# Performance work log

Measured on AMD Instinct MI355X. Metric: run time of the kernel, lower is better.

Reference implementation:

```python
import jax, jax.numpy as jnp
import numpy as np

T, B, D, H, O = 128, 256, 512, 1024, 1


def setup_inputs() -> dict:
    key = jax.random.key(0)
    ks = jax.random.split(key, 10)
    s_in = 1.0 / np.sqrt(D)
    s_h = 1.0 / np.sqrt(H)
    u = lambda k, shape, s: jax.random.uniform(k, shape, jnp.float32, -s, s)
    return {
        "inputs": jax.random.normal(ks[0], (T, B, D), jnp.float32),
        "hidden_state": jnp.zeros((1, B, H), jnp.float32),
        "cell_state": jnp.zeros((1, B, H), jnp.float32),
        "W1": u(ks[1], (H, D), s_in),
        "b1": u(ks[2], (H,), s_in),
        "W_ih": u(ks[3], (4 * H, H), s_h),
        "W_hh": u(ks[4], (4 * H, H), s_h),
        "b_ih": u(ks[5], (4 * H,), s_h),
        "b_hh": u(ks[6], (4 * H,), s_h),
        "W_out": u(ks[7], (O, H), s_h),
        "b_out": u(ks[8], (O,), s_h),
    }


def reference(inputs, hidden_state, cell_state, W1, b1, W_ih, W_hh, b_ih, b_hh, W_out, b_out):
    # first_layer + ReLU (dropout is identity in eval mode)
    x = jax.nn.relu(jnp.einsum("tbd,hd->tbh", inputs, W1) + b1)  # (T,B,H)
    # Precompute input contribution to all gates for every timestep.
    xg = jnp.einsum("tbh,gh->tbg", x, W_ih) + b_ih + b_hh  # (T,B,4H)
    h0 = hidden_state[0]
    c0 = cell_state[0]

    def step(carry, xg_t):
        h, c = carry
        g = xg_t + h @ W_hh.T  # (B,4H), PyTorch gate order i,f,g,o
        i, f, gg, o = jnp.split(g, 4, axis=-1)
        i = jax.nn.sigmoid(i)
        f = jax.nn.sigmoid(f)
        gg = jnp.tanh(gg)
        o = jax.nn.sigmoid(o)
        c = f * c + i * gg
        h = o * jnp.tanh(c)
        return (h, c), h

    (hT, cT), hs = jax.lax.scan(step, (h0, c0), xg)
    out = jnp.einsum("tbh,oh->tbo", hs, W_out) + b_out  # (T,B,O)
    return out, hT[None], cT[None]
```

## Files before the change

### kernel.cpp

```cpp
#include <hip/hip_runtime.h>
#include <hip/hip_bf16.h>
#include <math.h>


#define T_STEPS 128
#define BATCH   256
#define DIM     512
#define HID     1024
#define GATES   4096
#define FPAD    32

typedef __attribute__((ext_vector_type(8))) short short8;
typedef __attribute__((ext_vector_type(4))) float f4;
typedef __attribute__((ext_vector_type(4))) int i4;

__device__ __forceinline__ short f2bf(float f) {
    union { float f; unsigned u; } x; x.f = f;
    unsigned r = (x.u + 0x7fffu + ((x.u >> 16) & 1u)) >> 16;
    return (short)r;
}
__device__ __forceinline__ float bf2f(short s) {
    union { unsigned u; float f; } x; x.u = ((unsigned)(unsigned short)s) << 16;
    return x.f;
}
__device__ __forceinline__ float sigm(float x) { return 1.f / (1.f + __expf(-x)); }
__device__ __forceinline__ float tanh_fast(float x) { return 2.f / (1.f + __expf(-2.f * x)) - 1.f; }

__device__ __forceinline__ void gll16(const void* g, void* l) {
    __builtin_amdgcn_global_load_lds(
        (const __attribute__((address_space(1))) void*)g,
        (__attribute__((address_space(3))) void*)l, 16, 0, 0);
}
__device__ __forceinline__ void store16_wt(void* p, i4 v) {
    asm volatile("global_store_dwordx4 %0, %1, off sc0 sc1"
                 :: "v"(p), "v"(v) : "memory");
}

__global__ __launch_bounds__(256) void cvt_f32_bf16(const float* __restrict__ in,
                                                    short* __restrict__ out, int n4) {
    int i = blockIdx.x * 256 + threadIdx.x;
    if (i < n4) {
        float4 v = ((const float4*)in)[i];
        union { short s[4]; long long ll; } r;
        r.s[0] = f2bf(v.x); r.s[1] = f2bf(v.y); r.s[2] = f2bf(v.z); r.s[3] = f2bf(v.w);
        ((long long*)out)[i] = r.ll;
    }
}

__global__ __launch_bounds__(256) void cvt_h0_blocked(const float* __restrict__ h0,
                                                      short* __restrict__ dst) {
    int b = blockIdx.x, k0 = threadIdx.x * 4;
    float4 v = *(const float4*)&h0[(size_t)b * HID + k0];
    union { short s[4]; long long ll; } p;
    p.s[0] = f2bf(v.x); p.s[1] = f2bf(v.y); p.s[2] = f2bf(v.z); p.s[3] = f2bf(v.w);
    *(long long*)&dst[(k0 >> 3) * (BATCH * 8) + b * 8 + (k0 & 7)] = p.ll;
}

__global__ __launch_bounds__(256) void cvt_permute_rows(const float* __restrict__ in,
                                                        short* __restrict__ out) {
    int r = blockIdx.x;
    int hc = r >> 2, g = r & 3;
    const float* src = in + (size_t)(g * HID + hc) * HID;
    short* dst = out + (size_t)r * HID;
    int c = threadIdx.x * 4;
    float4 v = *(const float4*)&src[c];
    union { short s[4]; long long ll; } p;
    p.s[0] = f2bf(v.x); p.s[1] = f2bf(v.y); p.s[2] = f2bf(v.z); p.s[3] = f2bf(v.w);
    *(long long*)&dst[c] = p.ll;
}

__global__ __launch_bounds__(256) void bias_sum_perm(const float* __restrict__ a,
                                                     const float* __restrict__ b,
                                                     float* __restrict__ o) {
    int r = blockIdx.x * 256 + threadIdx.x;
    int hc = r >> 2, g = r & 3;
    int src = g * HID + hc;
    o[r] = a[src] + b[src];
}

__global__ __launch_bounds__(256) void copy_f32v4(const float* __restrict__ in,
                                                  float* __restrict__ out, int n4) {
    int i = blockIdx.x * 256 + threadIdx.x;
    if (i < n4) ((float4*)out)[i] = ((const float4*)in)[i];
}

__global__ __launch_bounds__(256) void zero_i32(int* __restrict__ p, int n) {
    for (int i = blockIdx.x * 256 + threadIdx.x; i < n; i += gridDim.x * 256)
        p[i] = 0;
}

__global__ __launch_bounds__(256) void gemm_bt2(const short* __restrict__ A,
                                                const short* __restrict__ B,
                                                const float* __restrict__ bias,
                                                short* __restrict__ C,
                                                int M, int N, int K, int do_relu) {
    __shared__ __align__(16) short As[2][128 * 64];
    __shared__ __align__(16) short Bs[2][128 * 64];
    const int tid = threadIdx.x, wave = tid >> 6, lane = tid & 63;
    const int wm = (wave >> 1) * 64, wn = (wave & 1) * 64;

    const int nwg = gridDim.x * gridDim.y;
    const int flat = blockIdx.y * gridDim.x + blockIdx.x;
    const int qq = nwg >> 3, rr = nwg & 7;
    const int xcd = flat & 7, oin = flat >> 3;
    const int swz = (xcd < rr ? xcd * (qq + 1) : rr * (qq + 1) + (xcd - rr) * qq) + oin;
    const int bm = (swz % gridDim.x) * 128, bn = (swz / gridDim.x) * 128;

#define STAGE2(bufi, kt)                                                       \
    {                                                                          \
        const int k0_ = (kt) * 64;                                             \
        _Pragma("unroll")                                                      \
        for (int u = 0; u < 4; ++u) {                                          \
            int r0 = wave * 32 + u * 8;                                        \
            int row = r0 + (lane >> 3);                                        \
            int kof = ((lane & 7) ^ (row & 7)) * 8;                            \
            gll16(&A[(size_t)(bm + row) * K + k0_ + kof], &As[bufi][r0 * 64]); \
            gll16(&B[(size_t)(bn + row) * K + k0_ + kof], &Bs[bufi][r0 * 64]); \
        }                                                                      \
    }

    f4 acc[4][4] = {};
    const int NT = K >> 6;

    STAGE2(0, 0)
    __syncthreads();

    int cur = 0;
    for (int kt = 0; kt < NT; ++kt) {
        if (kt + 1 < NT) STAGE2(cur ^ 1, kt + 1)

#pragma unroll
        for (int ks = 0; ks < 2; ++ks) {
            short8 af[4], bfr[4];
#pragma unroll
            for (int i = 0; i < 4; ++i) {
                int ra = wm + i * 16 + (lane & 15);
                int sa = (ks * 4 + (lane >> 4)) ^ (ra & 7);
                af[i] = *(const short8*)&As[cur][ra * 64 + sa * 8];
                int rb = wn + i * 16 + (lane & 15);
                int sb = (ks * 4 + (lane >> 4)) ^ (rb & 7);
                bfr[i] = *(const short8*)&Bs[cur][rb * 64 + sb * 8];
            }
            __builtin_amdgcn_s_setprio(1);
#pragma unroll
            for (int i = 0; i < 4; ++i)
#pragma unroll
                for (int j = 0; j < 4; ++j)
                    acc[i][j] = __builtin_amdgcn_mfma_f32_16x16x32_bf16(af[i], bfr[j], acc[i][j], 0, 0, 0);
            __builtin_amdgcn_s_setprio(0);
        }
        __syncthreads();
        cur ^= 1;
    }
#undef STAGE2

    const int lc = lane & 15, lr = (lane >> 4) * 4;
#pragma unroll
    for (int i = 0; i < 4; ++i) {
#pragma unroll
        for (int j = 0; j < 4; ++j) {
            int col = bn + wn + j * 16 + lc;
            float bv = bias[col];
#pragma unroll
            for (int r = 0; r < 4; ++r) {
                int row = bm + wm + i * 16 + lr + r;
                float v = acc[i][j][r] + bv;
                if (do_relu) v = fmaxf(v, 0.f);
                C[(size_t)row * N + col] = f2bf(v);
            }
        }
    }
}

__global__ __launch_bounds__(256) void lstm_persist(const short* __restrict__ Whh,
                                                    const short* __restrict__ xgc,
                                                    short* __restrict__ hist,
                                                    float* __restrict__ cf,
                                                    float* __restrict__ hT,
                                                    float* __restrict__ cT,
                                                    int* __restrict__ flags,
                                                    int* __restrict__ go,
                                                    int TC, int last) {
    __shared__ __align__(16) short Bf[32768];
    __shared__ __align__(16) short Ht[512];
    const int tid = threadIdx.x, w = tid >> 6, lane = tid & 63;
    const int bg = blockIdx.x >> 7, cg = blockIdx.x & 127;
    const int bb = bg * 64, hc0 = cg * 8;
    const int hcl = lane & 7, gp = (lane >> 3) & 1, q = lane >> 4;

#pragma unroll
    for (int i = 0; i < 16; ++i) {
        int p = w * 16 + i;
        int c = p >> 1, t = p & 1;
        gll16(&Whh[(size_t)((t * 2 + gp) * HID + hc0 + hcl) * HID + c * 32 + q * 8],
              &Bf[p * 512]);
    }

    const int rowb = bb + w * 16 + q * 4 + gp * 2;
    float creg[2];
#pragma unroll
    for (int e = 0; e < 2; ++e)
        creg[e] = cf[(size_t)(rowb + e) * HID + hc0 + hcl];

    __syncthreads();

    unsigned long long xw[2], xwn[2];
#pragma unroll
    for (int e = 0; e < 2; ++e)
        xw[e] = *(const unsigned long long*)&xgc[(size_t)(rowb + e) * GATES
                                                 + (hc0 + hcl) * 4];

#define ISSUE_A(buf, g)                                                        \
    _Pragma("unroll")                                                          \
    for (int i = 0; i < 8; ++i)                                                \
        buf[i] = *(const short8*)(abase + (size_t)((g) * 8 + i) * astr);

#define COMPUTE_A(buf, g)                                                      \
    __builtin_amdgcn_s_setprio(1);                                             \
    _Pragma("unroll")                                                          \
    for (int i = 0; i < 8; ++i) {                                              \
        short8 b0 = *(const short8*)&Bf[(((g) * 8 + i) * 2 + 0) * 512 + lane * 8]; \
        short8 b1 = *(const short8*)&Bf[(((g) * 8 + i) * 2 + 1) * 512 + lane * 8]; \
        acc0 = __builtin_amdgcn_mfma_f32_16x16x32_bf16(buf[i], b0, acc0, 0, 0, 0); \
        acc1 = __builtin_amdgcn_mfma_f32_16x16x32_bf16(buf[i], b1, acc1, 0, 0, 0); \
    }                                                                          \
    __builtin_amdgcn_s_setprio(0);

    for (int tt = 0; tt < TC; ++tt) {
        if (tt + 1 < TC) {
#pragma unroll
            for (int e = 0; e < 2; ++e)
                xwn[e] = *(const unsigned long long*)&xgc[(size_t)((tt + 1) * BATCH + rowb + e) * GATES
                                                          + (hc0 + hcl) * 4];
        }

        const short* abase = hist + (size_t)tt * BATCH * HID
                           + (size_t)q * (BATCH * 8) + (size_t)(bb + w * 16 + (lane & 15)) * 8;
        const size_t astr = (size_t)4 * (BATCH * 8);
        f4 acc0 = {}, acc1 = {};
        short8 ab0[8], ab1[8], ab2[8];
        ISSUE_A(ab0, 0)
        ISSUE_A(ab1, 1)
        ISSUE_A(ab2, 2)
        COMPUTE_A(ab0, 0)
        ISSUE_A(ab0, 3)
        COMPUTE_A(ab1, 1)
        COMPUTE_A(ab2, 2)
        COMPUTE_A(ab0, 3)

        float p0[4], p1[4];
#pragma unroll
        for (int r = 0; r < 4; ++r) {
            p0[r] = __shfl_xor(acc0[r], 8);
            p1[r] = __shfl_xor(acc1[r], 8);
        }

        int glast = last && (tt == TC - 1);
#pragma unroll
        for (int e = 0; e < 2; ++e) {
            int r = gp * 2 + e;
            size_t b = rowb + e;
            float gi = gp ? p0[r] : acc0[r];
            float gf = gp ? acc0[r] : p0[r];
            float gg = gp ? p1[r] : acc1[r];
            float go_ = gp ? acc1[r] : p1[r];
            gi += bf2f((short)(xw[e] & 0xffff));
            gf += bf2f((short)((xw[e] >> 16) & 0xffff));
            gg += bf2f((short)((xw[e] >> 32) & 0xffff));
            go_ += bf2f((short)((xw[e] >> 48) & 0xffff));
            float si = sigm(gi), sf = sigm(gf), tg = tanh_fast(gg), so = sigm(go_);
            float cn = sf * creg[e] + si * tg;
            float hv = so * tanh_fast(cn);
            creg[e] = cn;
            Ht[(w * 16 + q * 4 + gp * 2 + e) * 8 + hcl] = f2bf(hv);
            if (glast) {
                hT[b * HID + hc0 + hcl] = hv;
                cT[b * HID + hc0 + hcl] = cn;
            }
        }
        xw[0] = xwn[0]; xw[1] = xwn[1];
        __syncthreads();

        short* hn = hist + (size_t)(tt + 1) * BATCH * HID
                  + (size_t)cg * (BATCH * 8) + (size_t)bb * 8;
        if (tid < 64)
            store16_wt(&hn[tid * 8], *(const i4*)&Ht[tid * 8]);

        if (tt < TC - 1) {
            __syncthreads();
            const int base = (tt * 4 + bg) * 128 * FPAD;
            if (tid == 0)
                __hip_atomic_store(&flags[base + cg * FPAD], 1,
                                   __ATOMIC_RELAXED, __HIP_MEMORY_SCOPE_AGENT);
            if (cg == 0) {
                if (tid < 128) {
                    while (__hip_atomic_load(&flags[base + tid * FPAD],
                                             __ATOMIC_RELAXED, __HIP_MEMORY_SCOPE_AGENT) == 0)
                        __builtin_amdgcn_s_sleep(1);
                }
                __syncthreads();
                if (tid == 0)
                    __hip_atomic_store(&go[(tt * 4 + bg) * FPAD], 1,
                                       __ATOMIC_RELAXED, __HIP_MEMORY_SCOPE_AGENT);
            } else {
                if (tid == 0) {
                    while (__hip_atomic_load(&go[(tt * 4 + bg) * FPAD],
                                             __ATOMIC_RELAXED, __HIP_MEMORY_SCOPE_AGENT) == 0)
                        __builtin_amdgcn_s_sleep(1);
                }
                __syncthreads();
            }
        }
    }

#undef ISSUE_A
#undef COMPUTE_A

#pragma unroll
    for (int e = 0; e < 2; ++e)
        cf[(size_t)(rowb + e) * HID + hc0 + hcl] = creg[e];
}

__global__ __launch_bounds__(256) void out_head(const short* __restrict__ hs,
                                                const float* __restrict__ Wout,
                                                const float* __restrict__ bout,
                                                float* __restrict__ out) {
    int row = blockIdx.x * 4 + (threadIdx.x >> 6);
    int lane = threadIdx.x & 63;
    int tt = row >> 8, b = row & 255;
    const short* sb = hs + (size_t)(tt + 1) * BATCH * HID + b * 8;
    const float2* w2 = (const float2*)Wout;
    float s = 0.f;
#pragma unroll
    for (int j = 0; j < 8; ++j) {
        int m = j * 64 + lane;
        int pk = *(const int*)&sb[(size_t)(m >> 2) * (BATCH * 8) + 2 * (m & 3)];
        float2 wv = w2[m];
        union { unsigned u; float f; } lo, hi;
        lo.u = ((unsigned)pk) << 16;
        hi.u = ((unsigned)pk) & 0xffff0000u;
        s += lo.f * wv.x + hi.f * wv.y;
    }
#pragma unroll
    for (int off = 32; off; off >>= 1) s += __shfl_down(s, off);
    if (lane == 0) out[row] = s + bout[0];
}

extern "C" void kernel_launch(void* const* d_in, const int* in_sizes, int n_in,
                              void* d_out, int out_size, void* d_ws, size_t ws_size,
                              hipStream_t stream) {
    const float* inputs = (const float*)d_in[0];
    const float* h0     = (const float*)d_in[1];
    const float* c0     = (const float*)d_in[2];
    const float* W1     = (const float*)d_in[3];
    const float* b1     = (const float*)d_in[4];
    const float* W_ih   = (const float*)d_in[5];
    const float* W_hh   = (const float*)d_in[6];
    const float* b_ih   = (const float*)d_in[7];
    const float* b_hh   = (const float*)d_in[8];
    const float* W_out  = (const float*)d_in[9];
    const float* b_out  = (const float*)d_in[10];

    float* out = (float*)d_out;
    float* hT  = out + (size_t)T_STEPS * BATCH;
    float* cT  = hT + (size_t)BATCH * HID;

    char* base = (char*)d_ws;
    size_t off = 0;
    auto alloc = [&](size_t bytes) -> char* {
        char* q = base + off;
        off += (bytes + 255) & ~(size_t)255;
        return q;
    };
    short* W1b   = (short*)alloc((size_t)HID * DIM * 2);
    short* Wihb  = (short*)alloc((size_t)GATES * HID * 2);
    short* Whhb  = (short*)alloc((size_t)GATES * HID * 2);
    float* biasf = (float*)alloc((size_t)GATES * 4);
    float* cf    = (float*)alloc((size_t)BATCH * HID * 4);
    int*   flags = (int*)alloc((size_t)T_STEPS * 4 * 128 * FPAD * 4);
    int*   go    = (int*)alloc((size_t)T_STEPS * 4 * FPAD * 4);

    short* inb_a = (short*)alloc((size_t)T_STEPS * BATCH * DIM * 2);
    short* xb_a  = (short*)alloc((size_t)T_STEPS * BATCH * HID * 2);

    size_t per_t = (size_t)BATCH * GATES * 2 + (size_t)BATCH * HID * 2;
    int TC = 32;
    while (TC > 1 && off + (size_t)TC * per_t + (size_t)BATCH * HID * 2 + 65536 > ws_size)
        TC >>= 1;

    short* hhist = (short*)alloc((size_t)(TC + 1) * BATCH * HID * 2);
    short* xgb_c = (short*)alloc((size_t)TC * BATCH * GATES * 2);

    cvt_f32_bf16<<<(HID * DIM / 4 + 255) / 256, 256, 0, stream>>>(W1, W1b, HID * DIM / 4);
    cvt_permute_rows<<<GATES, 256, 0, stream>>>(W_ih, Wihb);
    cvt_f32_bf16<<<(GATES * HID / 4 + 255) / 256, 256, 0, stream>>>(W_hh, Whhb, GATES * HID / 4);
    bias_sum_perm<<<GATES / 256, 256, 0, stream>>>(b_ih, b_hh, biasf);
    cvt_h0_blocked<<<BATCH, 256, 0, stream>>>(h0, hhist);
    copy_f32v4<<<(BATCH * HID / 4 + 255) / 256, 256, 0, stream>>>(c0, cf, BATCH * HID / 4);
    zero_i32<<<512, 256, 0, stream>>>(flags, T_STEPS * 4 * 128 * FPAD + T_STEPS * 4 * FPAD);

    {
        int Ma = T_STEPS * BATCH;
        cvt_f32_bf16<<<(Ma * DIM / 4 + 255) / 256, 256, 0, stream>>>(
            inputs, inb_a, Ma * DIM / 4);
        gemm_bt2<<<dim3(Ma / 128, HID / 128), 256, 0, stream>>>(
            inb_a, W1b, b1, xb_a, Ma, HID, DIM, 1);
    }

    for (int t0 = 0; t0 < T_STEPS; t0 += TC) {
        int Mc = TC * BATCH;
        int last = (t0 + TC >= T_STEPS);
        gemm_bt2<<<dim3(Mc / 128, GATES / 128), 256, 0, stream>>>(
            xb_a + (size_t)t0 * BATCH * HID, Wihb, biasf, xgb_c,
            Mc, GATES, HID, 0);

        lstm_persist<<<512, 256, 0, stream>>>(Whhb, xgb_c, hhist, cf, hT, cT,
                                              flags + (size_t)t0 * 4 * 128 * FPAD,
                                              go + (size_t)t0 * 4 * FPAD,
                                              TC, last);

        out_head<<<TC * BATCH / 4, 256, 0, stream>>>(hhist, W_out, b_out,
                                                     out + (size_t)t0 * BATCH);
        copy_f32v4<<<(BATCH * HID * 2 / 16 + 255) / 256, 256, 0, stream>>>(
            (const float*)(hhist + (size_t)TC * BATCH * HID), (float*)hhist,
            BATCH * HID * 2 / 16);
    }
}
```

Measured before the change: 1.321 ms.

## Precompute all input-gate projections in one GEMM and keep full hidden history

```diff
diff --git a/kernel.cpp b/kernel.cpp
--- a/kernel.cpp
+++ b/kernel.cpp
@@ -380,16 +380,27 @@
     int*   flags = (int*)alloc((size_t)T_STEPS * 4 * 128 * FPAD * 4);
     int*   go    = (int*)alloc((size_t)T_STEPS * 4 * FPAD * 4);
 
-    short* inb_a = (short*)alloc((size_t)T_STEPS * BATCH * DIM * 2);
     short* xb_a  = (short*)alloc((size_t)T_STEPS * BATCH * HID * 2);
-
-    size_t per_t = (size_t)BATCH * GATES * 2 + (size_t)BATCH * HID * 2;
+    short* hhist = (short*)alloc((size_t)(T_STEPS + 1) * BATCH * HID * 2);
+
+    size_t xg_all_bytes = (size_t)T_STEPS * BATCH * GATES * 2;
+    size_t inb_bytes    = (size_t)T_STEPS * BATCH * DIM * 2;
+    int ALLX = (ws_size - off) >= (xg_all_bytes + 4096);
+    short *xgb = nullptr, *inb_a = nullptr;
     int TC = 32;
-    while (TC > 1 && off + (size_t)TC * per_t + (size_t)BATCH * HID * 2 + 65536 > ws_size)
-        TC >>= 1;
-
-    short* hhist = (short*)alloc((size_t)(TC + 1) * BATCH * HID * 2);
-    short* xgb_c = (short*)alloc((size_t)TC * BATCH * GATES * 2);
+    if (ALLX) {
+        xgb   = (short*)alloc(xg_all_bytes);
+        inb_a = xgb;
+    } else {
+        size_t per_c = (size_t)TC * BATCH * GATES * 2;
+        while (TC > 1 && off + (per_c > inb_bytes ? per_c : inb_bytes) + 4096 > ws_size) {
+            TC >>= 1;
+            per_c = (size_t)TC * BATCH * GATES * 2;
+        }
+        size_t region = per_c > inb_bytes ? per_c : inb_bytes;
+        xgb   = (short*)alloc(region);
+        inb_a = xgb;
+    }
 
     cvt_f32_bf16<<<(HID * DIM / 4 + 255) / 256, 256, 0, stream>>>(W1, W1b, HID * DIM / 4);
     cvt_permute_rows<<<GATES, 256, 0, stream>>>(W_ih, Wihb);
@@ -405,24 +416,32 @@
             inputs, inb_a, Ma * DIM / 4);
         gemm_bt2<<<dim3(Ma / 128, HID / 128), 256, 0, stream>>>(
             inb_a, W1b, b1, xb_a, Ma, HID, DIM, 1);
+        if (ALLX) {
+            gemm_bt2<<<dim3(Ma / 128, GATES / 128), 256, 0, stream>>>(
+                xb_a, Wihb, biasf, xgb, Ma, GATES, HID, 0);
+        }
     }
 
     for (int t0 = 0; t0 < T_STEPS; t0 += TC) {
-        int Mc = TC * BATCH;
         int last = (t0 + TC >= T_STEPS);
-        gemm_bt2<<<dim3(Mc / 128, GATES / 128), 256, 0, stream>>>(
-            xb_a + (size_t)t0 * BATCH * HID, Wihb, biasf, xgb_c,
-            Mc, GATES, HID, 0);
-
-        lstm_persist<<<512, 256, 0, stream>>>(Whhb, xgb_c, hhist, cf, hT, cT,
+        const short* xgc;
+        if (ALLX) {
+            xgc = xgb + (size_t)t0 * BATCH * GATES;
+        } else {
+            int Mc = TC * BATCH;
+            gemm_bt2<<<dim3(Mc / 128, GATES / 128), 256, 0, stream>>>(
+                xb_a + (size_t)t0 * BATCH * HID, Wihb, biasf, xgb,
+                Mc, GATES, HID, 0);
+            xgc = xgb;
+        }
+
+        lstm_persist<<<512, 256, 0, stream>>>(Whhb, xgc,
+                                              hhist + (size_t)t0 * BATCH * HID,
+                                              cf, hT, cT,
                                               flags + (size_t)t0 * 4 * 128 * FPAD,
                                               go + (size_t)t0 * 4 * FPAD,
                                               TC, last);
-
-        out_head<<<TC * BATCH / 4, 256, 0, stream>>>(hhist, W_out, b_out,
-                                                     out + (size_t)t0 * BATCH);
-        copy_f32v4<<<(BATCH * HID * 2 / 16 + 255) / 256, 256, 0, stream>>>(
-            (const float*)(hhist + (size_t)TC * BATCH * HID), (float*)hhist,
-            BATCH * HID * 2 / 16);
-    }
-}
+    }
+
+    out_head<<<T_STEPS * BATCH / 4, 256, 0, stream>>>(hhist, W_out, b_out, out);
+}
```

Measured after the change: 1.276 ms. 3.4% less time.
